# Kernel tuning notes

Hardware: AMD Instinct MI355X
Metric: run time of the kernel (lower is better)

## Reference

```python
import jax, jax.numpy as jnp
import numpy as np

WIN = (2, 7, 7)
SHIFT = (1, 3, 3)
D, H, W = 8, 56, 56
C, NH = 128, 4
B = 8
N = WIN[0] * WIN[1] * WIN[2]  # 98


def _relative_position_index():
    d, h, w = np.meshgrid(np.arange(WIN[0]), np.arange(WIN[1]), np.arange(WIN[2]), indexing='ij')
    coords = np.stack([d.ravel(), h.ravel(), w.ravel()])  # (3, N)
    rel = coords[:, :, None] - coords[:, None, :]  # (3, N, N)
    rel = rel.transpose(1, 2, 0).astype(np.int64)
    rel[:, :, 0] += WIN[0] - 1
    rel[:, :, 1] += WIN[1] - 1
    rel[:, :, 2] += WIN[2] - 1
    rel[:, :, 0] *= (2 * WIN[1] - 1) * (2 * WIN[2] - 1)
    rel[:, :, 1] *= 2 * WIN[2] - 1
    return rel.sum(-1).astype(np.int32)  # (N, N)


def _shift_mask():
    img = np.zeros((1, D, H, W, 1), dtype=np.float32)
    cnt = 0
    for ds in (slice(0, -WIN[0]), slice(-WIN[0], -SHIFT[0]), slice(-SHIFT[0], None)):
        for hs in (slice(0, -WIN[1]), slice(-WIN[1], -SHIFT[1]), slice(-SHIFT[1], None)):
            for ws in (slice(0, -WIN[2]), slice(-WIN[2], -SHIFT[2]), slice(-SHIFT[2], None)):
                img[:, ds, hs, ws, :] = cnt
                cnt += 1
    m = img.reshape(1, D // WIN[0], WIN[0], H // WIN[1], WIN[1], W // WIN[2], WIN[2], 1)
    m = m.transpose(0, 1, 3, 5, 2, 4, 6, 7).reshape(-1, N)  # (nW, N)
    diff = m[:, None, :] - m[:, :, None]
    return np.where(diff != 0, np.float32(-100.0), np.float32(0.0))  # (nW, N, N)


def setup_inputs() -> dict:
    key = jax.random.key(0)
    ks = jax.random.split(key, 6)
    nW = (D // WIN[0]) * (H // WIN[1]) * (W // WIN[2])  # 256
    B_ = B * nW  # 2048
    table_size = (2 * WIN[0] - 1) * (2 * WIN[1] - 1) * (2 * WIN[2] - 1)  # 507
    return {
        'x': jax.random.normal(ks[0], (B_, N, C), dtype=jnp.float32),
        'qkv_w': jax.random.normal(ks[1], (3 * C, C), dtype=jnp.float32) * 0.02,
        'qkv_b': jax.random.normal(ks[2], (3 * C,), dtype=jnp.float32) * 0.02,
        'rpb_table': jax.random.normal(ks[3], (table_size, NH), dtype=jnp.float32) * 0.02,
        'proj_w': jax.random.normal(ks[4], (C, C), dtype=jnp.float32) * 0.02,
        'proj_b': jax.random.normal(ks[5], (C,), dtype=jnp.float32) * 0.02,
        'rel_index': jnp.asarray(_relative_position_index()),
        'mask': jnp.asarray(_shift_mask()),
    }


def reference(x, qkv_w, qkv_b, rpb_table, proj_w, proj_b, rel_index, mask):
    B_, n, c = x.shape
    hd = c // NH
    scale = hd ** -0.5
    # qkv projection -> (B_, n, 3, NH, hd)
    qkv = (x @ qkv_w.T + qkv_b).reshape(B_, n, 3, NH, hd)
    qkv = jnp.transpose(qkv, (2, 0, 3, 1, 4))  # (3, B_, NH, n, hd)
    q, k, v = qkv[0], qkv[1], qkv[2]
    attn = jnp.einsum('bhnd,bhmd->bhnm', q * scale, k)  # (B_, NH, n, n)
    # relative position bias gather
    bias = rpb_table[rel_index[:n, :n].reshape(-1)].reshape(n, n, NH)
    attn = attn + jnp.transpose(bias, (2, 0, 1))[None]
    # shift mask add
    nW = mask.shape[0]
    attn = attn.reshape(B_ // nW, nW, NH, n, n) + mask[None, :, None]
    attn = jax.nn.softmax(attn.reshape(B_, NH, n, n), axis=-1)
    out = jnp.einsum('bhnm,bhmd->bhnd', attn, v)
    out = jnp.transpose(out, (0, 2, 1, 3)).reshape(B_, n, c)
    return out @ proj_w.T + proj_b
```

## Files before the change

kernel.cpp:

```cpp
#include <hip/hip_runtime.h>
#include <math.h>
#include <stdint.h>


#define LOG2E   1.4426950408889634f
#define MASKNEG (-144.26950408889634f)

typedef __attribute__((ext_vector_type(8))) short bf16x8;
typedef __attribute__((ext_vector_type(4))) float f32x4;

__device__ __forceinline__ unsigned short cvt1(float f) {
    __bf16 h = (__bf16)f;
    return __builtin_bit_cast(unsigned short, h);
}
__device__ __forceinline__ unsigned cvt2(float lo, float hi) {
    return (unsigned)cvt1(lo) | ((unsigned)cvt1(hi) << 16);
}

__device__ __forceinline__ int tok_code(int t) {
    int pd = t / 49;
    int r  = t - pd * 49;
    int ph = r / 7;
    int pw = r - ph * 7;
    return (pd >= 1 ? 1 : 0) | (ph >= 4 ? 2 : 0) | (pw >= 4 ? 4 : 0);
}

__device__ __forceinline__ float mterm(unsigned pk, int sh, unsigned ci, unsigned cls) {
    return ((((pk >> sh) & 255u) ^ ci) & cls) ? MASKNEG : 0.f;
}

__device__ __forceinline__ int swz(int row, int col) {
    return row * 128 + (((col >> 3) ^ (row & 7)) << 3) + (col & 7);
}
__device__ __forceinline__ int vswz(int row, int col) {
    return row * 128 + ((((col >> 3) ^ (row & 7) ^ ((row >> 2) & 3)) & 15) << 3) + (col & 7);
}

template<bool BIG>
__global__ void prep_kernel(const float* __restrict__ qkv_w,
                            const float* __restrict__ proj_w,
                            const float* __restrict__ rpb_table,
                            const int*   __restrict__ rel_index,
                            unsigned short* __restrict__ wqkv,
                            unsigned short* __restrict__ wproj,
                            void* __restrict__ btab) {
    int tid = blockIdx.x * blockDim.x + threadIdx.x;
    int stride = gridDim.x * blockDim.x;
    for (int i = tid; i < 384 * 128; i += stride) wqkv[i]  = cvt1(qkv_w[i]);
    for (int i = tid; i < 128 * 128; i += stride) wproj[i] = cvt1(proj_w[i]);
    if constexpr (BIG) {
        float* bm = (float*)btab;
        for (int idx = tid; idx < 32 * 112 * 112; idx += stride) {
            int ch = idx / 12544; int r = idx - ch * 12544;
            int i  = r / 112;     int j = r - i * 112;
            int cls = ch >> 2, h = ch & 3;
            float v;
            if (i < 98) {
                if (j < 98) {
                    float bias = rpb_table[rel_index[i * 98 + j] * 4 + h];
                    bool  msk  = (((unsigned)tok_code(i) ^ (unsigned)tok_code(j)) & (unsigned)cls) != 0;
                    v = bias * LOG2E + (msk ? MASKNEG : 0.f);
                } else v = -INFINITY;
            } else v = 0.f;
            bm[idx] = v;
        }
    } else {
        unsigned short* biasL = (unsigned short*)btab;
        for (int idx = tid; idx < 4 * 112 * 112; idx += stride) {
            int h = idx / 12544; int r = idx - h * 12544;
            int i = r / 112;     int j = r - i * 112;
            float v;
            if (i < 98) v = (j < 98) ? rpb_table[rel_index[i * 98 + j] * 4 + h] * LOG2E
                                     : -INFINITY;
            else v = 0.f;
            biasL[idx] = cvt1(v);
        }
    }
}

template<bool BIG>
__global__ __launch_bounds__(1024)
void swin_main(const float* __restrict__ x,
               const float* __restrict__ qkv_b,
               const float* __restrict__ proj_b,
               const unsigned short* __restrict__ wqkv,
               const unsigned short* __restrict__ wproj,
               const void* __restrict__ btab,
               float* __restrict__ out)
{
    extern __shared__ unsigned short lds[];
    unsigned short* q_lds  = lds;
    unsigned short* k_lds  = lds + 14336;
    unsigned short* vT_lds = lds + 28672;
    unsigned short* xo_lds = lds + 45056;
    unsigned short* p_lds  = lds + 59392;

    const int b    = blockIdx.x;
    const int tid  = threadIdx.x;
    const int wv   = tid >> 6;
    const int lane = tid & 63;
    const int l4   = lane >> 4;
    const int lc   = lane & 15;

    {
        int idx2 = tid * 2;
        int row  = idx2 >> 4;
        int c    = 112 + (idx2 & 15);
        *(unsigned int*)(vT_lds + vswz(row, c)) = 0u;
    }

    {
        const float* xb = x + (size_t)b * 12544;
        for (int idx = tid; idx < 3584; idx += 1024) {
            int tok = idx >> 5;
            int c   = (idx & 31) << 2;
            float4 v;
            if (tok < 98) v = *(const float4*)(xb + tok * 128 + c);
            else { v.x = 0.f; v.y = 0.f; v.z = 0.f; v.w = 0.f; }
            uint2 hv; hv.x = cvt2(v.x, v.y); hv.y = cvt2(v.z, v.w);
            *(uint2*)(xo_lds + swz(tok, c)) = hv;
        }
    }
    __syncthreads();

    {
        const int ct = wv;
        bf16x8 wf[4];
        f32x4  bias;
        const unsigned short* wrow = wqkv + (ct * 16 + lc) * 128;
#pragma unroll
        for (int kt = 0; kt < 4; ++kt) wf[kt] = *(const bf16x8*)(wrow + kt * 32 + l4 * 8);
#pragma unroll
        for (int r = 0; r < 4; ++r) bias[r] = qkv_b[ct * 16 + l4 * 4 + r];
        const bool  isq = (ct < 8);
        const float qs  = 0.17677669529663689f * LOG2E;
#pragma unroll
        for (int t = 0; t < 7; ++t) {
            bf16x8 xf[4];
#pragma unroll
            for (int kt = 0; kt < 4; ++kt)
                xf[kt] = *(bf16x8*)(xo_lds + swz(t * 16 + lc, kt * 32 + l4 * 8));
            f32x4 acc = bias;
#pragma unroll
            for (int kt = 0; kt < 4; ++kt)
                acc = __builtin_amdgcn_mfma_f32_16x16x32_bf16(wf[kt], xf[kt], acc, 0, 0, 0);
            int tok = t * 16 + lc;
            if (isq) {
                uint2 hv; hv.x = cvt2(acc[0] * qs, acc[1] * qs); hv.y = cvt2(acc[2] * qs, acc[3] * qs);
                *(uint2*)(q_lds + swz(tok, ct * 16 + l4 * 4)) = hv;
            } else {
                uint2 hv; hv.x = cvt2(acc[0], acc[1]); hv.y = cvt2(acc[2], acc[3]);
                *(uint2*)(k_lds + swz(tok, (ct - 8) * 16 + l4 * 4)) = hv;
            }
        }
        const int vd = (wv >> 1) * 16;
        bf16x8 wf2[4];
        const unsigned short* wrow2 = wqkv + (256 + vd + lc) * 128;
#pragma unroll
        for (int kt = 0; kt < 4; ++kt) wf2[kt] = *(const bf16x8*)(wrow2 + kt * 32 + l4 * 8);
        f32x4 bias2;
#pragma unroll
        for (int r = 0; r < 4; ++r) bias2[r] = qkv_b[256 + vd + l4 * 4 + r];
        const int t0 = (wv & 1) ? 4 : 0, t1 = (wv & 1) ? 7 : 4;
        for (int t = t0; t < t1; ++t) {
            bf16x8 xf[4];
#pragma unroll
            for (int kt = 0; kt < 4; ++kt)
                xf[kt] = *(bf16x8*)(xo_lds + swz(t * 16 + lc, kt * 32 + l4 * 8));
            f32x4 acc = bias2;
#pragma unroll
            for (int kt = 0; kt < 4; ++kt)
                acc = __builtin_amdgcn_mfma_f32_16x16x32_bf16(wf2[kt], xf[kt], acc, 0, 0, 0);
            int tok = t * 16 + lc;
            const int rb = vd + l4 * 4;
            vT_lds[vswz(rb + 0, tok)] = cvt1(acc[0]);
            vT_lds[vswz(rb + 1, tok)] = cvt1(acc[1]);
            vT_lds[vswz(rb + 2, tok)] = cvt1(acc[2]);
            vT_lds[vswz(rb + 3, tok)] = cvt1(acc[3]);
        }
    }
    __syncthreads();

    const int wi  = b & 255;
    const unsigned int cls =
        ((wi >> 6) == 3 ? 1u : 0u) | (((wi >> 3) & 7) == 7 ? 2u : 0u) | ((wi & 7) == 7 ? 4u : 0u);

    unsigned int jcp[7];
    if constexpr (!BIG) {
#pragma unroll
        for (int jt = 0; jt < 7; ++jt) {
            int jb = jt * 16 + l4 * 4;
            unsigned int p = 0;
#pragma unroll
            for (int r = 0; r < 4; ++r) p |= (unsigned)tok_code(jb + r < 98 ? jb + r : 0) << (8 * r);
            jcp[jt] = p;
        }
    }

    unsigned short* myP = p_lds + wv * 1280;

    for (int pass = 0; pass < 2; ++pass) {
        int task = wv + (pass << 4);
        if (task >= 28) break;
        int h  = task / 7;
        int it = task - h * 7;
        const int i_tok = it * 16 + lc;
        const bf16x8 qfrag = *(bf16x8*)(q_lds + swz(i_tok, h * 32 + l4 * 8));

        f32x4 cvec[7];
        if constexpr (BIG) {
            const float* bmrow = (const float*)btab + ((size_t)((int)cls * 4 + h) * 112 + i_tok) * 112;
#pragma unroll
            for (int jt = 0; jt < 7; ++jt)
                cvec[jt] = *(const f32x4*)(bmrow + jt * 16 + l4 * 4);
        } else {
            const unsigned short* brow = (const unsigned short*)btab + (h * 112 + i_tok) * 112;
            const unsigned int ci = (unsigned)tok_code(i_tok < 98 ? i_tok : 0);
            ushort4 bb[7];
#pragma unroll
            for (int jt = 0; jt < 7; ++jt)
                bb[jt] = *(const ushort4*)(brow + jt * 16 + l4 * 4);
#pragma unroll
            for (int jt = 0; jt < 7; ++jt) {
                cvec[jt][0] = __builtin_bit_cast(float, (unsigned)bb[jt].x << 16) + mterm(jcp[jt], 0,  ci, cls);
                cvec[jt][1] = __builtin_bit_cast(float, (unsigned)bb[jt].y << 16) + mterm(jcp[jt], 8,  ci, cls);
                cvec[jt][2] = __builtin_bit_cast(float, (unsigned)bb[jt].z << 16) + mterm(jcp[jt], 16, ci, cls);
                cvec[jt][3] = __builtin_bit_cast(float, (unsigned)bb[jt].w << 16) + mterm(jcp[jt], 24, ci, cls);
            }
        }

        f32x4 s[7];
#pragma unroll
        for (int jt = 0; jt < 7; ++jt) {
            bf16x8 kfrag = *(bf16x8*)(k_lds + swz(jt * 16 + lc, h * 32 + l4 * 8));
            s[jt] = __builtin_amdgcn_mfma_f32_16x16x32_bf16(kfrag, qfrag, cvec[jt], 0, 0, 0);
        }

        float m = -INFINITY;
#pragma unroll
        for (int jt = 0; jt < 7; ++jt)
            m = fmaxf(m, fmaxf(fmaxf(s[jt][0], s[jt][1]), fmaxf(s[jt][2], s[jt][3])));
        m = fmaxf(m, __shfl_xor(m, 16));
        m = fmaxf(m, __shfl_xor(m, 32));

        float lsum = 0.f;
        f32x4 o0 = {0.f, 0.f, 0.f, 0.f}, o1 = {0.f, 0.f, 0.f, 0.f};
#pragma unroll
        for (int jt4 = 0; jt4 < 4; ++jt4) {
            unsigned short* pb = myP + (jt4 & 1) * 640;
#pragma unroll
            for (int sub = 0; sub < 2; ++sub) {
                int jt = jt4 * 2 + sub;
                uint2 pv;
                if (jt < 7) {
                    float p0 = exp2f(s[jt][0] - m);
                    float p1 = exp2f(s[jt][1] - m);
                    float p2 = exp2f(s[jt][2] - m);
                    float p3 = exp2f(s[jt][3] - m);
                    lsum += (p0 + p1) + (p2 + p3);
                    pv.x = cvt2(p0, p1); pv.y = cvt2(p2, p3);
                } else {
                    pv.x = 0u; pv.y = 0u;
                }
                *(uint2*)(pb + lc * 40 + sub * 16 + l4 * 4) = pv;
            }
            bf16x8 pfrag = *(bf16x8*)(pb + lc * 40 + l4 * 8);
            bf16x8 va = *(bf16x8*)(vT_lds + vswz(h * 32 + lc,      jt4 * 32 + l4 * 8));
            bf16x8 vb = *(bf16x8*)(vT_lds + vswz(h * 32 + 16 + lc, jt4 * 32 + l4 * 8));
            o0 = __builtin_amdgcn_mfma_f32_16x16x32_bf16(va, pfrag, o0, 0, 0, 0);
            o1 = __builtin_amdgcn_mfma_f32_16x16x32_bf16(vb, pfrag, o1, 0, 0, 0);
        }
        lsum += __shfl_xor(lsum, 16);
        lsum += __shfl_xor(lsum, 32);

        float inv = 1.0f / lsum;
        uint2 h0, h1;
        h0.x = cvt2(o0[0] * inv, o0[1] * inv); h0.y = cvt2(o0[2] * inv, o0[3] * inv);
        h1.x = cvt2(o1[0] * inv, o1[1] * inv); h1.y = cvt2(o1[2] * inv, o1[3] * inv);
        *(uint2*)(xo_lds + swz(i_tok, h * 32 + l4 * 4)) = h0;
        *(uint2*)(xo_lds + swz(i_tok, h * 32 + 16 + l4 * 4)) = h1;
    }
    __syncthreads();

    {
        const int ct = wv >> 1;
        bf16x8 pw[4];
#pragma unroll
        for (int kt = 0; kt < 4; ++kt)
            pw[kt] = *(const bf16x8*)(wproj + (ct * 16 + lc) * 128 + kt * 32 + l4 * 8);
        f32x4 pbias;
#pragma unroll
        for (int r = 0; r < 4; ++r) pbias[r] = proj_b[ct * 16 + l4 * 4 + r];

        float* ob = out + (size_t)b * 12544;
        const int t0 = (wv & 1) ? 4 : 0, t1 = (wv & 1) ? 7 : 4;
        for (int t = t0; t < t1; ++t) {
            f32x4 acc = pbias;
#pragma unroll
            for (int kt = 0; kt < 4; ++kt) {
                bf16x8 of = *(bf16x8*)(xo_lds + swz(t * 16 + lc, kt * 32 + l4 * 8));
                acc = __builtin_amdgcn_mfma_f32_16x16x32_bf16(pw[kt], of, acc, 0, 0, 0);
            }
            int tok = t * 16 + lc;
            if (tok < 98) {
                float4 st; st.x = acc[0]; st.y = acc[1]; st.z = acc[2]; st.w = acc[3];
                *(float4*)(ob + tok * 128 + ct * 16 + l4 * 4) = st;
            }
        }
    }
}

extern "C" void kernel_launch(void* const* d_in, const int* in_sizes, int n_in,
                              void* d_out, int out_size, void* d_ws, size_t ws_size,
                              hipStream_t stream) {
    const float* x       = (const float*)d_in[0];
    const float* qkv_w   = (const float*)d_in[1];
    const float* qkv_b   = (const float*)d_in[2];
    const float* rpb_tab = (const float*)d_in[3];
    const float* proj_w  = (const float*)d_in[4];
    const float* proj_b  = (const float*)d_in[5];
    const int*   rel_idx = (const int*)d_in[6];

    unsigned short* wqkv  = (unsigned short*)d_ws;
    unsigned short* wproj = (unsigned short*)((char*)d_ws + 98304);
    void*           btab  = (void*)((char*)d_ws + 131072);
    float*          out   = (float*)d_out;

    const bool big = ws_size >= (size_t)(131072 + 32 * 112 * 112 * 4);
    const int LDS_BYTES = 159744;

    if (big) {
        hipLaunchKernelGGL((prep_kernel<true>), dim3(512), dim3(256), 0, stream,
                           qkv_w, proj_w, rpb_tab, rel_idx, wqkv, wproj, btab);
        (void)hipFuncSetAttribute((const void*)(swin_main<true>),
                                  hipFuncAttributeMaxDynamicSharedMemorySize, LDS_BYTES);
        hipLaunchKernelGGL((swin_main<true>), dim3(2048), dim3(1024), LDS_BYTES, stream,
                           x, qkv_b, proj_b, wqkv, wproj, btab, out);
    } else {
        hipLaunchKernelGGL((prep_kernel<false>), dim3(512), dim3(256), 0, stream,
                           qkv_w, proj_w, rpb_tab, rel_idx, wqkv, wproj, btab);
        (void)hipFuncSetAttribute((const void*)(swin_main<false>),
                                  hipFuncAttributeMaxDynamicSharedMemorySize, LDS_BYTES);
        hipLaunchKernelGGL((swin_main<false>), dim3(2048), dim3(1024), LDS_BYTES, stream,
                           x, qkv_b, proj_b, wqkv, wproj, btab, out);
    }
}
```

Measured before the change: 137.9 us.

## Switch attention core to 32x32x16 MFMA with register-resident P via permlane32 swap

Rewrites the attention stage so each of the 16 waves handles one head and one 32-token query tile with 32x32x16 bf16 MFMAs instead of 16x16 tiles over two passes. The softmax probabilities stay in registers and are rearranged with v_permlane32_swap rather than bounced through an LDS P buffer, which removes the P scratch area and cuts dynamic LDS. The bias/mask table is re-laid out in the prep kernel to match the 32x32 accumulator layout, and a unified swizzle replaces the two earlier ones. It pads to 128 tokens rather than 112, adding some wasted MFMA work, and depends on the permlane swap instruction and an exact accumulator layout being right.

```diff
diff --git a/kernel.cpp b/kernel.cpp
--- a/kernel.cpp
+++ b/kernel.cpp
@@ -6,8 +6,10 @@
 #define LOG2E   1.4426950408889634f
 #define MASKNEG (-144.26950408889634f)
 
-typedef __attribute__((ext_vector_type(8))) short bf16x8;
-typedef __attribute__((ext_vector_type(4))) float f32x4;
+typedef __attribute__((ext_vector_type(8)))  short    bf16x8;
+typedef __attribute__((ext_vector_type(4)))  float    f32x4;
+typedef __attribute__((ext_vector_type(16))) float    f32x16;
+typedef __attribute__((ext_vector_type(4)))  unsigned uint32x4;
 
 __device__ __forceinline__ unsigned short cvt1(float f) {
     __bf16 h = (__bf16)f;
@@ -15,6 +17,10 @@
 }
 __device__ __forceinline__ unsigned cvt2(float lo, float hi) {
     return (unsigned)cvt1(lo) | ((unsigned)cvt1(hi) << 16);
+}
+
+__device__ __forceinline__ void pswap(unsigned &a, unsigned &b) {
+    asm volatile("v_permlane32_swap_b32 %0, %1" : "+v"(a), "+v"(b));
 }
 
 __device__ __forceinline__ int tok_code(int t) {
@@ -25,15 +31,8 @@
     return (pd >= 1 ? 1 : 0) | (ph >= 4 ? 2 : 0) | (pw >= 4 ? 4 : 0);
 }
 
-__device__ __forceinline__ float mterm(unsigned pk, int sh, unsigned ci, unsigned cls) {
-    return ((((pk >> sh) & 255u) ^ ci) & cls) ? MASKNEG : 0.f;
-}
-
-__device__ __forceinline__ int swz(int row, int col) {
-    return row * 128 + (((col >> 3) ^ (row & 7)) << 3) + (col & 7);
-}
-__device__ __forceinline__ int vswz(int row, int col) {
-    return row * 128 + ((((col >> 3) ^ (row & 7) ^ ((row >> 2) & 3)) & 15) << 3) + (col & 7);
+__device__ __forceinline__ int swz2(int row, int col) {
+    return row * 128 + ((((col >> 3) ^ (row & 7) ^ ((row >> 3) & 3)) & 15) << 3) + (col & 7);
 }
 
 template<bool BIG>
@@ -50,30 +49,44 @@
     for (int i = tid; i < 128 * 128; i += stride) wproj[i] = cvt1(proj_w[i]);
     if constexpr (BIG) {
         float* bm = (float*)btab;
-        for (int idx = tid; idx < 32 * 112 * 112; idx += stride) {
-            int ch = idx / 12544; int r = idx - ch * 12544;
-            int i  = r / 112;     int j = r - i * 112;
-            int cls = ch >> 2, h = ch & 3;
+        for (int idx = tid; idx < 524288; idx += stride) {
+            int e  = idx & 3;
+            int il = (idx >> 2) & 31;
+            int hi = (idx >> 7) & 1;
+            int q  = (idx >> 8) & 3;
+            int jt = (idx >> 10) & 3;
+            int it = (idx >> 12) & 3;
+            int h  = (idx >> 14) & 3;
+            int cl = (idx >> 16);
+            int i = it * 32 + il;
+            int j = jt * 32 + q * 8 + hi * 4 + e;
             float v;
-            if (i < 98) {
-                if (j < 98) {
-                    float bias = rpb_table[rel_index[i * 98 + j] * 4 + h];
-                    bool  msk  = (((unsigned)tok_code(i) ^ (unsigned)tok_code(j)) & (unsigned)cls) != 0;
-                    v = bias * LOG2E + (msk ? MASKNEG : 0.f);
-                } else v = -INFINITY;
-            } else v = 0.f;
+            if (j >= 98) v = -INFINITY;
+            else if (i >= 98) v = 0.f;
+            else {
+                float bias = rpb_table[rel_index[i * 98 + j] * 4 + h];
+                bool  msk  = (((unsigned)tok_code(i) ^ (unsigned)tok_code(j)) & (unsigned)cl) != 0;
+                v = bias * LOG2E + (msk ? MASKNEG : 0.f);
+            }
             bm[idx] = v;
         }
     } else {
-        unsigned short* biasL = (unsigned short*)btab;
-        for (int idx = tid; idx < 4 * 112 * 112; idx += stride) {
-            int h = idx / 12544; int r = idx - h * 12544;
-            int i = r / 112;     int j = r - i * 112;
+        unsigned short* bm = (unsigned short*)btab;
+        for (int idx = tid; idx < 65536; idx += stride) {
+            int e  = idx & 3;
+            int il = (idx >> 2) & 31;
+            int hi = (idx >> 7) & 1;
+            int q  = (idx >> 8) & 3;
+            int jt = (idx >> 10) & 3;
+            int it = (idx >> 12) & 3;
+            int h  = (idx >> 14) & 3;
+            int i = it * 32 + il;
+            int j = jt * 32 + q * 8 + hi * 4 + e;
             float v;
-            if (i < 98) v = (j < 98) ? rpb_table[rel_index[i * 98 + j] * 4 + h] * LOG2E
-                                     : -INFINITY;
-            else v = 0.f;
-            biasL[idx] = cvt1(v);
+            if (j >= 98) v = -INFINITY;
+            else if (i >= 98) v = 0.f;
+            else v = rpb_table[rel_index[i * 98 + j] * 4 + h] * LOG2E;
+            bm[idx] = cvt1(v);
         }
     }
 }
@@ -93,7 +106,6 @@
     unsigned short* k_lds  = lds + 14336;
     unsigned short* vT_lds = lds + 28672;
     unsigned short* xo_lds = lds + 45056;
-    unsigned short* p_lds  = lds + 59392;
 
     const int b    = blockIdx.x;
     const int tid  = threadIdx.x;
@@ -106,7 +118,7 @@
         int idx2 = tid * 2;
         int row  = idx2 >> 4;
         int c    = 112 + (idx2 & 15);
-        *(unsigned int*)(vT_lds + vswz(row, c)) = 0u;
+        *(unsigned int*)(vT_lds + swz2(row, c)) = 0u;
     }
 
     {
@@ -118,7 +130,7 @@
             if (tok < 98) v = *(const float4*)(xb + tok * 128 + c);
             else { v.x = 0.f; v.y = 0.f; v.z = 0.f; v.w = 0.f; }
             uint2 hv; hv.x = cvt2(v.x, v.y); hv.y = cvt2(v.z, v.w);
-            *(uint2*)(xo_lds + swz(tok, c)) = hv;
+            *(uint2*)(xo_lds + swz2(tok, c)) = hv;
         }
     }
     __syncthreads();
@@ -139,7 +151,7 @@
             bf16x8 xf[4];
 #pragma unroll
             for (int kt = 0; kt < 4; ++kt)
-                xf[kt] = *(bf16x8*)(xo_lds + swz(t * 16 + lc, kt * 32 + l4 * 8));
+                xf[kt] = *(bf16x8*)(xo_lds + swz2(t * 16 + lc, kt * 32 + l4 * 8));
             f32x4 acc = bias;
 #pragma unroll
             for (int kt = 0; kt < 4; ++kt)
@@ -147,10 +159,10 @@
             int tok = t * 16 + lc;
             if (isq) {
                 uint2 hv; hv.x = cvt2(acc[0] * qs, acc[1] * qs); hv.y = cvt2(acc[2] * qs, acc[3] * qs);
-                *(uint2*)(q_lds + swz(tok, ct * 16 + l4 * 4)) = hv;
+                *(uint2*)(q_lds + swz2(tok, ct * 16 + l4 * 4)) = hv;
             } else {
                 uint2 hv; hv.x = cvt2(acc[0], acc[1]); hv.y = cvt2(acc[2], acc[3]);
-                *(uint2*)(k_lds + swz(tok, (ct - 8) * 16 + l4 * 4)) = hv;
+                *(uint2*)(k_lds + swz2(tok, (ct - 8) * 16 + l4 * 4)) = hv;
             }
         }
         const int vd = (wv >> 1) * 16;
@@ -166,17 +178,17 @@
             bf16x8 xf[4];
 #pragma unroll
             for (int kt = 0; kt < 4; ++kt)
-                xf[kt] = *(bf16x8*)(xo_lds + swz(t * 16 + lc, kt * 32 + l4 * 8));
+                xf[kt] = *(bf16x8*)(xo_lds + swz2(t * 16 + lc, kt * 32 + l4 * 8));
             f32x4 acc = bias2;
 #pragma unroll
             for (int kt = 0; kt < 4; ++kt)
                 acc = __builtin_amdgcn_mfma_f32_16x16x32_bf16(wf2[kt], xf[kt], acc, 0, 0, 0);
             int tok = t * 16 + lc;
             const int rb = vd + l4 * 4;
-            vT_lds[vswz(rb + 0, tok)] = cvt1(acc[0]);
-            vT_lds[vswz(rb + 1, tok)] = cvt1(acc[1]);
-            vT_lds[vswz(rb + 2, tok)] = cvt1(acc[2]);
-            vT_lds[vswz(rb + 3, tok)] = cvt1(acc[3]);
+            vT_lds[swz2(rb + 0, tok)] = cvt1(acc[0]);
+            vT_lds[swz2(rb + 1, tok)] = cvt1(acc[1]);
+            vT_lds[swz2(rb + 2, tok)] = cvt1(acc[2]);
+            vT_lds[swz2(rb + 3, tok)] = cvt1(acc[3]);
         }
     }
     __syncthreads();
@@ -184,101 +196,102 @@
     const int wi  = b & 255;
     const unsigned int cls =
         ((wi >> 6) == 3 ? 1u : 0u) | (((wi >> 3) & 7) == 7 ? 2u : 0u) | ((wi & 7) == 7 ? 4u : 0u);
-
-    unsigned int jcp[7];
-    if constexpr (!BIG) {
-#pragma unroll
-        for (int jt = 0; jt < 7; ++jt) {
-            int jb = jt * 16 + l4 * 4;
-            unsigned int p = 0;
-#pragma unroll
-            for (int r = 0; r < 4; ++r) p |= (unsigned)tok_code(jb + r < 98 ? jb + r : 0) << (8 * r);
-            jcp[jt] = p;
-        }
-    }
-
-    unsigned short* myP = p_lds + wv * 1280;
-
-    for (int pass = 0; pass < 2; ++pass) {
-        int task = wv + (pass << 4);
-        if (task >= 28) break;
-        int h  = task / 7;
-        int it = task - h * 7;
-        const int i_tok = it * 16 + lc;
-        const bf16x8 qfrag = *(bf16x8*)(q_lds + swz(i_tok, h * 32 + l4 * 8));
-
-        f32x4 cvec[7];
+    {
+        const int il  = lane & 31;
+        const int hi2 = lane >> 5;
+        const int h     = wv >> 2;
+        const int itile = wv & 3;
+        const int i_tok = itile * 32 + il;
+
+        f32x16 S[4];
         if constexpr (BIG) {
-            const float* bmrow = (const float*)btab + ((size_t)((int)cls * 4 + h) * 112 + i_tok) * 112;
-#pragma unroll
-            for (int jt = 0; jt < 7; ++jt)
-                cvec[jt] = *(const f32x4*)(bmrow + jt * 16 + l4 * 4);
+            const float* tb = (const float*)btab
+                + (((size_t)(cls * 4 + h) * 4 + itile) * 4) * 1024 + hi2 * 128 + il * 4;
+#pragma unroll
+            for (int jt = 0; jt < 4; ++jt)
+#pragma unroll
+                for (int q = 0; q < 4; ++q) {
+                    f32x4 v = *(const f32x4*)(tb + (jt * 8 + q * 2) * 128);
+                    S[jt][q * 4 + 0] = v[0]; S[jt][q * 4 + 1] = v[1];
+                    S[jt][q * 4 + 2] = v[2]; S[jt][q * 4 + 3] = v[3];
+                }
         } else {
-            const unsigned short* brow = (const unsigned short*)btab + (h * 112 + i_tok) * 112;
-            const unsigned int ci = (unsigned)tok_code(i_tok < 98 ? i_tok : 0);
-            ushort4 bb[7];
-#pragma unroll
-            for (int jt = 0; jt < 7; ++jt)
-                bb[jt] = *(const ushort4*)(brow + jt * 16 + l4 * 4);
-#pragma unroll
-            for (int jt = 0; jt < 7; ++jt) {
-                cvec[jt][0] = __builtin_bit_cast(float, (unsigned)bb[jt].x << 16) + mterm(jcp[jt], 0,  ci, cls);
-                cvec[jt][1] = __builtin_bit_cast(float, (unsigned)bb[jt].y << 16) + mterm(jcp[jt], 8,  ci, cls);
-                cvec[jt][2] = __builtin_bit_cast(float, (unsigned)bb[jt].z << 16) + mterm(jcp[jt], 16, ci, cls);
-                cvec[jt][3] = __builtin_bit_cast(float, (unsigned)bb[jt].w << 16) + mterm(jcp[jt], 24, ci, cls);
-            }
-        }
-
-        f32x4 s[7];
-#pragma unroll
-        for (int jt = 0; jt < 7; ++jt) {
-            bf16x8 kfrag = *(bf16x8*)(k_lds + swz(jt * 16 + lc, h * 32 + l4 * 8));
-            s[jt] = __builtin_amdgcn_mfma_f32_16x16x32_bf16(kfrag, qfrag, cvec[jt], 0, 0, 0);
-        }
-
-        float m = -INFINITY;
-#pragma unroll
-        for (int jt = 0; jt < 7; ++jt)
-            m = fmaxf(m, fmaxf(fmaxf(s[jt][0], s[jt][1]), fmaxf(s[jt][2], s[jt][3])));
-        m = fmaxf(m, __shfl_xor(m, 16));
+            const unsigned short* tb = (const unsigned short*)btab
+                + ((h * 4 + itile) * 4) * 1024 + hi2 * 128 + il * 4;
+            const unsigned int ci = (unsigned)tok_code(i_tok);
+#pragma unroll
+            for (int jt = 0; jt < 4; ++jt)
+#pragma unroll
+                for (int q = 0; q < 4; ++q) {
+                    ushort4 bb = *(const ushort4*)(tb + (jt * 8 + q * 2) * 128);
+#pragma unroll
+                    for (int e = 0; e < 4; ++e) {
+                        unsigned short us = (e == 0) ? bb.x : (e == 1) ? bb.y : (e == 2) ? bb.z : bb.w;
+                        int j = jt * 32 + q * 8 + hi2 * 4 + e;
+                        float mv = (((unsigned)tok_code(j) ^ ci) & cls) ? MASKNEG : 0.f;
+                        S[jt][q * 4 + e] = __builtin_bit_cast(float, (unsigned)us << 16) + mv;
+                    }
+                }
+        }
+
+        bf16x8 qfa = *(bf16x8*)(q_lds + swz2(i_tok, h * 32 + hi2 * 8));
+        bf16x8 qfb = *(bf16x8*)(q_lds + swz2(i_tok, h * 32 + 16 + hi2 * 8));
+#pragma unroll
+        for (int jt = 0; jt < 4; ++jt) {
+            bf16x8 ka = *(bf16x8*)(k_lds + swz2(jt * 32 + il, h * 32 + hi2 * 8));
+            bf16x8 kb = *(bf16x8*)(k_lds + swz2(jt * 32 + il, h * 32 + 16 + hi2 * 8));
+            S[jt] = __builtin_amdgcn_mfma_f32_32x32x16_bf16(ka, qfa, S[jt], 0, 0, 0);
+            S[jt] = __builtin_amdgcn_mfma_f32_32x32x16_bf16(kb, qfb, S[jt], 0, 0, 0);
+        }
+
+        float m = S[0][0];
+#pragma unroll
+        for (int jt = 0; jt < 4; ++jt)
+#pragma unroll
+            for (int r = 0; r < 16; ++r)
+                if (!(jt == 0 && r == 0)) m = fmaxf(m, S[jt][r]);
         m = fmaxf(m, __shfl_xor(m, 32));
 
-        float lsum = 0.f;
-        f32x4 o0 = {0.f, 0.f, 0.f, 0.f}, o1 = {0.f, 0.f, 0.f, 0.f};
-#pragma unroll
-        for (int jt4 = 0; jt4 < 4; ++jt4) {
-            unsigned short* pb = myP + (jt4 & 1) * 640;
-#pragma unroll
-            for (int sub = 0; sub < 2; ++sub) {
-                int jt = jt4 * 2 + sub;
-                uint2 pv;
-                if (jt < 7) {
-                    float p0 = exp2f(s[jt][0] - m);
-                    float p1 = exp2f(s[jt][1] - m);
-                    float p2 = exp2f(s[jt][2] - m);
-                    float p3 = exp2f(s[jt][3] - m);
-                    lsum += (p0 + p1) + (p2 + p3);
-                    pv.x = cvt2(p0, p1); pv.y = cvt2(p2, p3);
-                } else {
-                    pv.x = 0u; pv.y = 0u;
-                }
-                *(uint2*)(pb + lc * 40 + sub * 16 + l4 * 4) = pv;
-            }
-            bf16x8 pfrag = *(bf16x8*)(pb + lc * 40 + l4 * 8);
-            bf16x8 va = *(bf16x8*)(vT_lds + vswz(h * 32 + lc,      jt4 * 32 + l4 * 8));
-            bf16x8 vb = *(bf16x8*)(vT_lds + vswz(h * 32 + 16 + lc, jt4 * 32 + l4 * 8));
-            o0 = __builtin_amdgcn_mfma_f32_16x16x32_bf16(va, pfrag, o0, 0, 0, 0);
-            o1 = __builtin_amdgcn_mfma_f32_16x16x32_bf16(vb, pfrag, o1, 0, 0, 0);
-        }
-        lsum += __shfl_xor(lsum, 16);
-        lsum += __shfl_xor(lsum, 32);
-
-        float inv = 1.0f / lsum;
-        uint2 h0, h1;
-        h0.x = cvt2(o0[0] * inv, o0[1] * inv); h0.y = cvt2(o0[2] * inv, o0[3] * inv);
-        h1.x = cvt2(o1[0] * inv, o1[1] * inv); h1.y = cvt2(o1[2] * inv, o1[3] * inv);
-        *(uint2*)(xo_lds + swz(i_tok, h * 32 + l4 * 4)) = h0;
-        *(uint2*)(xo_lds + swz(i_tok, h * 32 + 16 + l4 * 4)) = h1;
+        float l = 0.f;
+        unsigned dw[4][8];
+#pragma unroll
+        for (int jt = 0; jt < 4; ++jt)
+#pragma unroll
+            for (int d = 0; d < 8; ++d) {
+                float p0 = exp2f(S[jt][2 * d]     - m);
+                float p1 = exp2f(S[jt][2 * d + 1] - m);
+                l += p0 + p1;
+                dw[jt][d] = cvt2(p0, p1);
+            }
+        l += __shfl_xor(l, 32);
+
+#pragma unroll
+        for (int jt = 0; jt < 4; ++jt) {
+            pswap(dw[jt][0], dw[jt][2]);
+            pswap(dw[jt][1], dw[jt][3]);
+            pswap(dw[jt][4], dw[jt][6]);
+            pswap(dw[jt][5], dw[jt][7]);
+        }
+
+        f32x16 O = {0.f,0.f,0.f,0.f,0.f,0.f,0.f,0.f,0.f,0.f,0.f,0.f,0.f,0.f,0.f,0.f};
+#pragma unroll
+        for (int jt = 0; jt < 4; ++jt)
+#pragma unroll
+            for (int p = 0; p < 2; ++p) {
+                bf16x8 vf = *(bf16x8*)(vT_lds + swz2(h * 32 + il, jt * 32 + p * 16 + hi2 * 8));
+                uint32x4 pu = { dw[jt][p * 4 + 0], dw[jt][p * 4 + 1],
+                                dw[jt][p * 4 + 2], dw[jt][p * 4 + 3] };
+                O = __builtin_amdgcn_mfma_f32_32x32x16_bf16(
+                        vf, __builtin_bit_cast(bf16x8, pu), O, 0, 0, 0);
+            }
+
+        const float inv = 1.0f / l;
+#pragma unroll
+        for (int rr = 0; rr < 8; ++rr) {
+            int r = rr * 2;
+            int d = (r & 3) + 8 * (r >> 2) + 4 * hi2;
+            *(unsigned*)(xo_lds + swz2(i_tok, h * 32 + d)) = cvt2(O[r] * inv, O[r + 1] * inv);
+        }
     }
     __syncthreads();
 
@@ -298,7 +311,7 @@
             f32x4 acc = pbias;
 #pragma unroll
             for (int kt = 0; kt < 4; ++kt) {
-                bf16x8 of = *(bf16x8*)(xo_lds + swz(t * 16 + lc, kt * 32 + l4 * 8));
+                bf16x8 of = *(bf16x8*)(xo_lds + swz2(t * 16 + lc, kt * 32 + l4 * 8));
                 acc = __builtin_amdgcn_mfma_f32_16x16x32_bf16(pw[kt], of, acc, 0, 0, 0);
             }
             int tok = t * 16 + lc;
@@ -326,8 +339,8 @@
     void*           btab  = (void*)((char*)d_ws + 131072);
     float*          out   = (float*)d_out;
 
-    const bool big = ws_size >= (size_t)(131072 + 32 * 112 * 112 * 4);
-    const int LDS_BYTES = 159744;
+    const bool big = ws_size >= (size_t)(131072 + 524288 * 4);
+    const int LDS_BYTES = 122880;
 
     if (big) {
         hipLaunchKernelGGL((prep_kernel<true>), dim3(512), dim3(256), 0, stream,
```

Measured after the change: 151.1 us. +9.5%, slower.

## Split fused Swin attention into per-head-group attention and separate projection kernels

Applied to the files above, without the earlier changes.

Adds a new path that splits each window across two 512-thread blocks (two heads each), using 32x32x16 MFMA for QK and PV with a precomputed bias/mask table laid out in accumulator order, and permlane32 swaps to repack P. The attention output goes to a bf16 workspace, and a separate tiled kernel applies the output projection. The aim is to cut LDS per block (so several blocks fit per CU) and to get better MFMA efficiency. In exchange it adds an extra global round trip for the intermediate plus a third launch, and it needs a much larger workspace, so it only runs if ws_size is big enough.

```diff
diff --git a/kernel.cpp b/kernel.cpp
--- a/kernel.cpp
+++ b/kernel.cpp
@@ -6,8 +6,10 @@
 #define LOG2E   1.4426950408889634f
 #define MASKNEG (-144.26950408889634f)
 
-typedef __attribute__((ext_vector_type(8))) short bf16x8;
-typedef __attribute__((ext_vector_type(4))) float f32x4;
+typedef __attribute__((ext_vector_type(8)))  short    bf16x8;
+typedef __attribute__((ext_vector_type(4)))  float    f32x4;
+typedef __attribute__((ext_vector_type(16))) float    f32x16;
+typedef __attribute__((ext_vector_type(4)))  unsigned uint32x4;
 
 __device__ __forceinline__ unsigned short cvt1(float f) {
     __bf16 h = (__bf16)f;
@@ -16,7 +18,9 @@
 __device__ __forceinline__ unsigned cvt2(float lo, float hi) {
     return (unsigned)cvt1(lo) | ((unsigned)cvt1(hi) << 16);
 }
-
+__device__ __forceinline__ void pswap(unsigned &a, unsigned &b) {
+    asm volatile("v_permlane32_swap_b32 %0, %1" : "+v"(a), "+v"(b));
+}
 __device__ __forceinline__ int tok_code(int t) {
     int pd = t / 49;
     int r  = t - pd * 49;
@@ -24,26 +28,302 @@
     int pw = r - ph * 7;
     return (pd >= 1 ? 1 : 0) | (ph >= 4 ? 2 : 0) | (pw >= 4 ? 4 : 0);
 }
-
 __device__ __forceinline__ float mterm(unsigned pk, int sh, unsigned ci, unsigned cls) {
     return ((((pk >> sh) & 255u) ^ ci) & cls) ? MASKNEG : 0.f;
 }
-
-__device__ __forceinline__ int swz(int row, int col) {
+__device__ __forceinline__ int swz2(int row, int col) {
+    return row * 128 + ((((col >> 3) ^ (row & 7) ^ ((row >> 3) & 3)) & 15) << 3) + (col & 7);
+}
+__device__ __forceinline__ int swz64(int row, int col) {
+    return row * 64 + ((((col >> 3) ^ (row & 7)) & 7) << 3) + (col & 7);
+}
+__device__ __forceinline__ int swzA(int row, int col) {
     return row * 128 + (((col >> 3) ^ (row & 7)) << 3) + (col & 7);
 }
 __device__ __forceinline__ int vswz(int row, int col) {
     return row * 128 + ((((col >> 3) ^ (row & 7) ^ ((row >> 2) & 3)) & 15) << 3) + (col & 7);
 }
 
+__global__ void pipe_prep(const float* __restrict__ qkv_w,
+                          const float* __restrict__ proj_w,
+                          const float* __restrict__ rpb_table,
+                          const int*   __restrict__ rel_index,
+                          unsigned short* __restrict__ wqkv,
+                          unsigned short* __restrict__ wproj,
+                          float* __restrict__ bm) {
+    int tid = blockIdx.x * blockDim.x + threadIdx.x;
+    int stride = gridDim.x * blockDim.x;
+    for (int i = tid; i < 384 * 128; i += stride) wqkv[i]  = cvt1(qkv_w[i]);
+    for (int i = tid; i < 128 * 128; i += stride) wproj[i] = cvt1(proj_w[i]);
+    for (int idx = tid; idx < 524288; idx += stride) {
+        int e  = idx & 3;
+        int il = (idx >> 2) & 31;
+        int hi = (idx >> 7) & 1;
+        int q  = (idx >> 8) & 3;
+        int jt = (idx >> 10) & 3;
+        int it = (idx >> 12) & 3;
+        int h  = (idx >> 14) & 3;
+        int cl = (idx >> 16);
+        int i = it * 32 + il;
+        int j = jt * 32 + q * 8 + hi * 4 + e;
+        float v;
+        if (j >= 98) v = -INFINITY;
+        else if (i >= 98) v = 0.f;
+        else {
+            float bias = rpb_table[rel_index[i * 98 + j] * 4 + h];
+            bool  msk  = (((unsigned)tok_code(i) ^ (unsigned)tok_code(j)) & (unsigned)cl) != 0;
+            v = bias * LOG2E + (msk ? MASKNEG : 0.f);
+        }
+        bm[idx] = v;
+    }
+}
+
+__global__ __launch_bounds__(512, 4)
+void swin_qkattn(const float* __restrict__ x,
+                 const float* __restrict__ qkv_b,
+                 const unsigned short* __restrict__ wqkv,
+                 const float* __restrict__ bm,
+                 unsigned* __restrict__ O_ws)
+{
+    extern __shared__ unsigned short lds[];
+    unsigned short* x_lds  = lds;
+    unsigned short* q_lds  = lds + 14336;
+    unsigned short* k_lds  = lds + 21504;
+    unsigned short* vT_lds = lds + 28672;
+
+    const int bid  = blockIdx.x;
+    const int b    = bid >> 1;
+    const int g    = bid & 1;
+    const int tid  = threadIdx.x;
+    const int wv   = tid >> 6;
+    const int lane = tid & 63;
+    const int l4   = lane >> 4;
+    const int lc   = lane & 15;
+
+    {
+        int idx2 = tid * 2;
+        int row  = idx2 >> 4;
+        int c    = 112 + (idx2 & 15);
+        *(unsigned*)(vT_lds + swz2(row, c)) = 0u;
+    }
+    {
+        const float* xb = x + (size_t)b * 12544;
+        for (int idx = tid; idx < 3584; idx += 512) {
+            int tok = idx >> 5;
+            int c   = (idx & 31) << 2;
+            float4 v;
+            if (tok < 98) v = *(const float4*)(xb + tok * 128 + c);
+            else { v.x = 0.f; v.y = 0.f; v.z = 0.f; v.w = 0.f; }
+            uint2 hv; hv.x = cvt2(v.x, v.y); hv.y = cvt2(v.z, v.w);
+            *(uint2*)(x_lds + swz2(tok, c)) = hv;
+        }
+    }
+    __syncthreads();
+
+    {
+        const bool isq = (wv < 4);
+        const int  lt  = wv & 3;
+        const int  wbase = (isq ? 0 : 128) + g * 64 + lt * 16;
+        bf16x8 wf[4];
+        const unsigned short* wrow = wqkv + (wbase + lc) * 128;
+#pragma unroll
+        for (int kt = 0; kt < 4; ++kt) wf[kt] = *(const bf16x8*)(wrow + kt * 32 + l4 * 8);
+        f32x4 bias;
+#pragma unroll
+        for (int r = 0; r < 4; ++r) bias[r] = qkv_b[wbase + l4 * 4 + r];
+        const float qs = 0.17677669529663689f * LOG2E;
+        unsigned short* dst = isq ? q_lds : k_lds;
+#pragma unroll
+        for (int t = 0; t < 7; ++t) {
+            bf16x8 xf[4];
+#pragma unroll
+            for (int kt = 0; kt < 4; ++kt)
+                xf[kt] = *(bf16x8*)(x_lds + swz2(t * 16 + lc, kt * 32 + l4 * 8));
+            f32x4 acc = bias;
+#pragma unroll
+            for (int kt = 0; kt < 4; ++kt)
+                acc = __builtin_amdgcn_mfma_f32_16x16x32_bf16(wf[kt], xf[kt], acc, 0, 0, 0);
+            int tok = t * 16 + lc;
+            uint2 hv;
+            if (isq) { hv.x = cvt2(acc[0] * qs, acc[1] * qs); hv.y = cvt2(acc[2] * qs, acc[3] * qs); }
+            else     { hv.x = cvt2(acc[0], acc[1]);           hv.y = cvt2(acc[2], acc[3]); }
+            *(uint2*)(dst + swz64(tok, lt * 16 + l4 * 4)) = hv;
+        }
+        const int vd = (wv >> 1) * 16;
+        bf16x8 wf2[4];
+        const unsigned short* wrow2 = wqkv + (256 + g * 64 + vd + lc) * 128;
+#pragma unroll
+        for (int kt = 0; kt < 4; ++kt) wf2[kt] = *(const bf16x8*)(wrow2 + kt * 32 + l4 * 8);
+        f32x4 bias2;
+#pragma unroll
+        for (int r = 0; r < 4; ++r) bias2[r] = qkv_b[256 + g * 64 + vd + l4 * 4 + r];
+        const int t0 = (wv & 1) ? 4 : 0, t1 = (wv & 1) ? 7 : 4;
+        for (int t = t0; t < t1; ++t) {
+            bf16x8 xf[4];
+#pragma unroll
+            for (int kt = 0; kt < 4; ++kt)
+                xf[kt] = *(bf16x8*)(x_lds + swz2(t * 16 + lc, kt * 32 + l4 * 8));
+            f32x4 acc = bias2;
+#pragma unroll
+            for (int kt = 0; kt < 4; ++kt)
+                acc = __builtin_amdgcn_mfma_f32_16x16x32_bf16(wf2[kt], xf[kt], acc, 0, 0, 0);
+            int tok = t * 16 + lc;
+            const int rb = vd + l4 * 4;
+            vT_lds[swz2(rb + 0, tok)] = cvt1(acc[0]);
+            vT_lds[swz2(rb + 1, tok)] = cvt1(acc[1]);
+            vT_lds[swz2(rb + 2, tok)] = cvt1(acc[2]);
+            vT_lds[swz2(rb + 3, tok)] = cvt1(acc[3]);
+        }
+    }
+    __syncthreads();
+
+    {
+        const int wi  = b & 255;
+        const unsigned cls =
+            ((wi >> 6) == 3 ? 1u : 0u) | (((wi >> 3) & 7) == 7 ? 2u : 0u) | ((wi & 7) == 7 ? 4u : 0u);
+        const int il  = lane & 31;
+        const int hi2 = lane >> 5;
+        const int hl    = wv >> 2;
+        const int itile = wv & 3;
+        const int hg    = g * 2 + hl;
+        const int i_tok = itile * 32 + il;
+
+        f32x16 S[4];
+        const float* tb = bm + (((size_t)(cls * 4 + hg) * 4 + itile) * 4) * 1024 + hi2 * 128 + il * 4;
+#pragma unroll
+        for (int jt = 0; jt < 4; ++jt)
+#pragma unroll
+            for (int q = 0; q < 4; ++q) {
+                f32x4 v = *(const f32x4*)(tb + (jt * 8 + q * 2) * 128);
+                S[jt][q * 4 + 0] = v[0]; S[jt][q * 4 + 1] = v[1];
+                S[jt][q * 4 + 2] = v[2]; S[jt][q * 4 + 3] = v[3];
+            }
+
+        bf16x8 qfa = *(bf16x8*)(q_lds + swz64(i_tok, hl * 32 + hi2 * 8));
+        bf16x8 qfb = *(bf16x8*)(q_lds + swz64(i_tok, hl * 32 + 16 + hi2 * 8));
+#pragma unroll
+        for (int jt = 0; jt < 4; ++jt) {
+            bf16x8 ka = *(bf16x8*)(k_lds + swz64(jt * 32 + il, hl * 32 + hi2 * 8));
+            bf16x8 kb = *(bf16x8*)(k_lds + swz64(jt * 32 + il, hl * 32 + 16 + hi2 * 8));
+            S[jt] = __builtin_amdgcn_mfma_f32_32x32x16_bf16(ka, qfa, S[jt], 0, 0, 0);
+            S[jt] = __builtin_amdgcn_mfma_f32_32x32x16_bf16(kb, qfb, S[jt], 0, 0, 0);
+        }
+
+        float m = S[0][0];
+#pragma unroll
+        for (int jt = 0; jt < 4; ++jt)
+#pragma unroll
+            for (int r = 0; r < 16; ++r)
+                if (!(jt == 0 && r == 0)) m = fmaxf(m, S[jt][r]);
+        m = fmaxf(m, __shfl_xor(m, 32));
+
+        float l = 0.f;
+        unsigned dw[4][8];
+#pragma unroll
+        for (int jt = 0; jt < 4; ++jt)
+#pragma unroll
+            for (int d = 0; d < 8; ++d) {
+                float p0 = exp2f(S[jt][2 * d]     - m);
+                float p1 = exp2f(S[jt][2 * d + 1] - m);
+                l += p0 + p1;
+                dw[jt][d] = cvt2(p0, p1);
+            }
+        l += __shfl_xor(l, 32);
+
+#pragma unroll
+        for (int jt = 0; jt < 4; ++jt) {
+            pswap(dw[jt][0], dw[jt][2]);
+            pswap(dw[jt][1], dw[jt][3]);
+            pswap(dw[jt][4], dw[jt][6]);
+            pswap(dw[jt][5], dw[jt][7]);
+        }
+
+        f32x16 O = {0.f,0.f,0.f,0.f,0.f,0.f,0.f,0.f,0.f,0.f,0.f,0.f,0.f,0.f,0.f,0.f};
+#pragma unroll
+        for (int jt = 0; jt < 4; ++jt)
+#pragma unroll
+            for (int p = 0; p < 2; ++p) {
+                bf16x8 vf = *(bf16x8*)(vT_lds + swz2(hl * 32 + il, jt * 32 + p * 16 + hi2 * 8));
+                uint32x4 pu = { dw[jt][p * 4 + 0], dw[jt][p * 4 + 1],
+                                dw[jt][p * 4 + 2], dw[jt][p * 4 + 3] };
+                O = __builtin_amdgcn_mfma_f32_32x32x16_bf16(
+                        vf, __builtin_bit_cast(bf16x8, pu), O, 0, 0, 0);
+            }
+
+        const float inv = 1.0f / l;
+#pragma unroll
+        for (int rr = 0; rr < 8; ++rr) {
+            int r = rr * 2;
+            int d = (r & 3) + 8 * (r >> 2) + 4 * hi2;
+            *(unsigned*)(x_lds + swz2(i_tok, hl * 32 + d)) = cvt2(O[r] * inv, O[r + 1] * inv);
+        }
+    }
+    __syncthreads();
+
+    {
+        for (int idx = tid; idx < 3136; idx += 512) {
+            int tok = idx >> 5;
+            int c   = (idx & 31) * 2;
+            unsigned v = *(unsigned*)(x_lds + swz2(tok, c));
+            O_ws[((size_t)b * 98 + tok) * 64 + g * 32 + (idx & 31)] = v;
+        }
+    }
+}
+
+__global__ __launch_bounds__(256)
+void swin_proj(const unsigned short* __restrict__ O_ws,
+               const unsigned short* __restrict__ wproj,
+               const float* __restrict__ proj_b,
+               float* __restrict__ out)
+{
+    __shared__ unsigned short ot[8192];
+    const int tid  = threadIdx.x;
+    const int wv   = tid >> 6;
+    const int lane = tid & 63;
+    const int l4   = lane >> 4;
+    const int lc   = lane & 15;
+    const size_t T0 = (size_t)blockIdx.x * 64;
+
+    for (int idx = tid; idx < 1024; idx += 256) {
+        int tok_l = idx >> 4;
+        int c     = (idx & 15) << 3;
+        bf16x8 v = *(const bf16x8*)(O_ws + (T0 + tok_l) * 128 + c);
+        *(bf16x8*)(ot + swz2(tok_l, c)) = v;
+    }
+    __syncthreads();
+
+#pragma unroll
+    for (int pass = 0; pass < 2; ++pass) {
+        const int ct = wv + pass * 4;
+        bf16x8 pw[4];
+#pragma unroll
+        for (int kt = 0; kt < 4; ++kt)
+            pw[kt] = *(const bf16x8*)(wproj + (ct * 16 + lc) * 128 + kt * 32 + l4 * 8);
+        f32x4 pbias;
+#pragma unroll
+        for (int r = 0; r < 4; ++r) pbias[r] = proj_b[ct * 16 + l4 * 4 + r];
+#pragma unroll
+        for (int t = 0; t < 4; ++t) {
+            f32x4 acc = pbias;
+#pragma unroll
+            for (int kt = 0; kt < 4; ++kt) {
+                bf16x8 of = *(bf16x8*)(ot + swz2(t * 16 + lc, kt * 32 + l4 * 8));
+                acc = __builtin_amdgcn_mfma_f32_16x16x32_bf16(pw[kt], of, acc, 0, 0, 0);
+            }
+            float4 st; st.x = acc[0]; st.y = acc[1]; st.z = acc[2]; st.w = acc[3];
+            *(float4*)(out + (T0 + t * 16 + lc) * 128 + ct * 16 + l4 * 4) = st;
+        }
+    }
+}
+
 template<bool BIG>
-__global__ void prep_kernel(const float* __restrict__ qkv_w,
-                            const float* __restrict__ proj_w,
-                            const float* __restrict__ rpb_table,
-                            const int*   __restrict__ rel_index,
-                            unsigned short* __restrict__ wqkv,
-                            unsigned short* __restrict__ wproj,
-                            void* __restrict__ btab) {
+__global__ void fb_prep(const float* __restrict__ qkv_w,
+                        const float* __restrict__ proj_w,
+                        const float* __restrict__ rpb_table,
+                        const int*   __restrict__ rel_index,
+                        unsigned short* __restrict__ wqkv,
+                        unsigned short* __restrict__ wproj,
+                        void* __restrict__ btab) {
     int tid = blockIdx.x * blockDim.x + threadIdx.x;
     int stride = gridDim.x * blockDim.x;
     for (int i = tid; i < 384 * 128; i += stride) wqkv[i]  = cvt1(qkv_w[i]);
@@ -80,13 +360,13 @@
 
 template<bool BIG>
 __global__ __launch_bounds__(1024)
-void swin_main(const float* __restrict__ x,
-               const float* __restrict__ qkv_b,
-               const float* __restrict__ proj_b,
-               const unsigned short* __restrict__ wqkv,
-               const unsigned short* __restrict__ wproj,
-               const void* __restrict__ btab,
-               float* __restrict__ out)
+void fb_main(const float* __restrict__ x,
+             const float* __restrict__ qkv_b,
+             const float* __restrict__ proj_b,
+             const unsigned short* __restrict__ wqkv,
+             const unsigned short* __restrict__ wproj,
+             const void* __restrict__ btab,
+             float* __restrict__ out)
 {
     extern __shared__ unsigned short lds[];
     unsigned short* q_lds  = lds;
@@ -106,9 +386,8 @@
         int idx2 = tid * 2;
         int row  = idx2 >> 4;
         int c    = 112 + (idx2 & 15);
-        *(unsigned int*)(vT_lds + vswz(row, c)) = 0u;
-    }
-
+        *(unsigned*)(vT_lds + vswz(row, c)) = 0u;
+    }
     {
         const float* xb = x + (size_t)b * 12544;
         for (int idx = tid; idx < 3584; idx += 1024) {
@@ -118,11 +397,10 @@
             if (tok < 98) v = *(const float4*)(xb + tok * 128 + c);
             else { v.x = 0.f; v.y = 0.f; v.z = 0.f; v.w = 0.f; }
             uint2 hv; hv.x = cvt2(v.x, v.y); hv.y = cvt2(v.z, v.w);
-            *(uint2*)(xo_lds + swz(tok, c)) = hv;
+            *(uint2*)(xo_lds + swzA(tok, c)) = hv;
         }
     }
     __syncthreads();
-
     {
         const int ct = wv;
         bf16x8 wf[4];
@@ -139,7 +417,7 @@
             bf16x8 xf[4];
 #pragma unroll
             for (int kt = 0; kt < 4; ++kt)
-                xf[kt] = *(bf16x8*)(xo_lds + swz(t * 16 + lc, kt * 32 + l4 * 8));
+                xf[kt] = *(bf16x8*)(xo_lds + swzA(t * 16 + lc, kt * 32 + l4 * 8));
             f32x4 acc = bias;
 #pragma unroll
             for (int kt = 0; kt < 4; ++kt)
@@ -147,10 +425,10 @@
             int tok = t * 16 + lc;
             if (isq) {
                 uint2 hv; hv.x = cvt2(acc[0] * qs, acc[1] * qs); hv.y = cvt2(acc[2] * qs, acc[3] * qs);
-                *(uint2*)(q_lds + swz(tok, ct * 16 + l4 * 4)) = hv;
+                *(uint2*)(q_lds + swzA(tok, ct * 16 + l4 * 4)) = hv;
             } else {
                 uint2 hv; hv.x = cvt2(acc[0], acc[1]); hv.y = cvt2(acc[2], acc[3]);
-                *(uint2*)(k_lds + swz(tok, (ct - 8) * 16 + l4 * 4)) = hv;
+                *(uint2*)(k_lds + swzA(tok, (ct - 8) * 16 + l4 * 4)) = hv;
             }
         }
         const int vd = (wv >> 1) * 16;
@@ -166,7 +444,7 @@
             bf16x8 xf[4];
 #pragma unroll
             for (int kt = 0; kt < 4; ++kt)
-                xf[kt] = *(bf16x8*)(xo_lds + swz(t * 16 + lc, kt * 32 + l4 * 8));
+                xf[kt] = *(bf16x8*)(xo_lds + swzA(t * 16 + lc, kt * 32 + l4 * 8));
             f32x4 acc = bias2;
 #pragma unroll
             for (int kt = 0; kt < 4; ++kt)
@@ -182,21 +460,20 @@
     __syncthreads();
 
     const int wi  = b & 255;
-    const unsigned int cls =
+    const unsigned cls =
         ((wi >> 6) == 3 ? 1u : 0u) | (((wi >> 3) & 7) == 7 ? 2u : 0u) | ((wi & 7) == 7 ? 4u : 0u);
 
-    unsigned int jcp[7];
+    unsigned jcp[7];
     if constexpr (!BIG) {
 #pragma unroll
         for (int jt = 0; jt < 7; ++jt) {
             int jb = jt * 16 + l4 * 4;
-            unsigned int p = 0;
+            unsigned p = 0;
 #pragma unroll
             for (int r = 0; r < 4; ++r) p |= (unsigned)tok_code(jb + r < 98 ? jb + r : 0) << (8 * r);
             jcp[jt] = p;
         }
     }
-
     unsigned short* myP = p_lds + wv * 1280;
 
     for (int pass = 0; pass < 2; ++pass) {
@@ -205,7 +482,7 @@
         int h  = task / 7;
         int it = task - h * 7;
         const int i_tok = it * 16 + lc;
-        const bf16x8 qfrag = *(bf16x8*)(q_lds + swz(i_tok, h * 32 + l4 * 8));
+        const bf16x8 qfrag = *(bf16x8*)(q_lds + swzA(i_tok, h * 32 + l4 * 8));
 
         f32x4 cvec[7];
         if constexpr (BIG) {
@@ -215,7 +492,7 @@
                 cvec[jt] = *(const f32x4*)(bmrow + jt * 16 + l4 * 4);
         } else {
             const unsigned short* brow = (const unsigned short*)btab + (h * 112 + i_tok) * 112;
-            const unsigned int ci = (unsigned)tok_code(i_tok < 98 ? i_tok : 0);
+            const unsigned ci = (unsigned)tok_code(i_tok < 98 ? i_tok : 0);
             ushort4 bb[7];
 #pragma unroll
             for (int jt = 0; jt < 7; ++jt)
@@ -232,7 +509,7 @@
         f32x4 s[7];
 #pragma unroll
         for (int jt = 0; jt < 7; ++jt) {
-            bf16x8 kfrag = *(bf16x8*)(k_lds + swz(jt * 16 + lc, h * 32 + l4 * 8));
+            bf16x8 kfrag = *(bf16x8*)(k_lds + swzA(jt * 16 + lc, h * 32 + l4 * 8));
             s[jt] = __builtin_amdgcn_mfma_f32_16x16x32_bf16(kfrag, qfrag, cvec[jt], 0, 0, 0);
         }
 
@@ -277,11 +554,10 @@
         uint2 h0, h1;
         h0.x = cvt2(o0[0] * inv, o0[1] * inv); h0.y = cvt2(o0[2] * inv, o0[3] * inv);
         h1.x = cvt2(o1[0] * inv, o1[1] * inv); h1.y = cvt2(o1[2] * inv, o1[3] * inv);
-        *(uint2*)(xo_lds + swz(i_tok, h * 32 + l4 * 4)) = h0;
-        *(uint2*)(xo_lds + swz(i_tok, h * 32 + 16 + l4 * 4)) = h1;
+        *(uint2*)(xo_lds + swzA(i_tok, h * 32 + l4 * 4)) = h0;
+        *(uint2*)(xo_lds + swzA(i_tok, h * 32 + 16 + l4 * 4)) = h1;
     }
     __syncthreads();
-
     {
         const int ct = wv >> 1;
         bf16x8 pw[4];
@@ -298,7 +574,7 @@
             f32x4 acc = pbias;
 #pragma unroll
             for (int kt = 0; kt < 4; ++kt) {
-                bf16x8 of = *(bf16x8*)(xo_lds + swz(t * 16 + lc, kt * 32 + l4 * 8));
+                bf16x8 of = *(bf16x8*)(xo_lds + swzA(t * 16 + lc, kt * 32 + l4 * 8));
                 acc = __builtin_amdgcn_mfma_f32_16x16x32_bf16(pw[kt], of, acc, 0, 0, 0);
             }
             int tok = t * 16 + lc;
@@ -326,22 +602,31 @@
     void*           btab  = (void*)((char*)d_ws + 131072);
     float*          out   = (float*)d_out;
 
-    const bool big = ws_size >= (size_t)(131072 + 32 * 112 * 112 * 4);
-    const int LDS_BYTES = 159744;
-
-    if (big) {
-        hipLaunchKernelGGL((prep_kernel<true>), dim3(512), dim3(256), 0, stream,
+    const size_t PIPE_WS = 131072u + 2097152u + (size_t)200704 * 128 * 2;
+    if (ws_size >= PIPE_WS) {
+        float*    bm   = (float*)btab;
+        unsigned* O_ws = (unsigned*)((char*)d_ws + 131072 + 2097152);
+        hipLaunchKernelGGL(pipe_prep, dim3(512), dim3(256), 0, stream,
+                           qkv_w, proj_w, rpb_tab, rel_idx, wqkv, wproj, bm);
+        (void)hipFuncSetAttribute((const void*)swin_qkattn,
+                                  hipFuncAttributeMaxDynamicSharedMemorySize, 73728);
+        hipLaunchKernelGGL(swin_qkattn, dim3(4096), dim3(512), 73728, stream,
+                           x, qkv_b, wqkv, bm, O_ws);
+        hipLaunchKernelGGL(swin_proj, dim3(3136), dim3(256), 0, stream,
+                           (const unsigned short*)O_ws, wproj, proj_b, out);
+    } else if (ws_size >= (size_t)(131072 + 32 * 112 * 112 * 4)) {
+        hipLaunchKernelGGL((fb_prep<true>), dim3(512), dim3(256), 0, stream,
                            qkv_w, proj_w, rpb_tab, rel_idx, wqkv, wproj, btab);
-        (void)hipFuncSetAttribute((const void*)(swin_main<true>),
-                                  hipFuncAttributeMaxDynamicSharedMemorySize, LDS_BYTES);
-        hipLaunchKernelGGL((swin_main<true>), dim3(2048), dim3(1024), LDS_BYTES, stream,
+        (void)hipFuncSetAttribute((const void*)(fb_main<true>),
+                                  hipFuncAttributeMaxDynamicSharedMemorySize, 159744);
+        hipLaunchKernelGGL((fb_main<true>), dim3(2048), dim3(1024), 159744, stream,
                            x, qkv_b, proj_b, wqkv, wproj, btab, out);
     } else {
-        hipLaunchKernelGGL((prep_kernel<false>), dim3(512), dim3(256), 0, stream,
+        hipLaunchKernelGGL((fb_prep<false>), dim3(512), dim3(256), 0, stream,
                            qkv_w, proj_w, rpb_tab, rel_idx, wqkv, wproj, btab);
-        (void)hipFuncSetAttribute((const void*)(swin_main<false>),
-                                  hipFuncAttributeMaxDynamicSharedMemorySize, LDS_BYTES);
-        hipLaunchKernelGGL((swin_main<false>), dim3(2048), dim3(1024), LDS_BYTES, stream,
+        (void)hipFuncSetAttribute((const void*)(fb_main<false>),
+                                  hipFuncAttributeMaxDynamicSharedMemorySize, 159744);
+        hipLaunchKernelGGL((fb_main<false>), dim3(2048), dim3(1024), 159744, stream,
                            x, qkv_b, proj_b, wqkv, wproj, btab, out);
     }
 }
```

Result: slower. 154.0 us (+11.6%).
